# Optimization experiments

Hardware: AMD Instinct MI355X
Metric: run time of the kernel (lower is better)

## Reference

```python
import jax, jax.numpy as jnp
import numpy as np

C, N, D = 4, 300000, 128

def setup_inputs() -> dict:
    key = jax.random.key(0)
    k1, k2, k3 = jax.random.split(key, 3)
    hs = jax.random.normal(k1, (C, N, D), dtype=jnp.float32)
    # Linear(att_dim, att_dim) params (torch Linear: y = x @ W.T + b)
    W = jax.random.normal(k2, (D, D), dtype=jnp.float32) * (1.0 / np.sqrt(D))
    b = jnp.zeros((D,), dtype=jnp.float32)
    # meta attention parameter [nchannel, att_dim]
    meta_att = jax.random.normal(k3, (C, D), dtype=jnp.float32) * 0.1
    return {"hs": hs, "W": W, "b": b, "meta_att": meta_att, "nnode": N}

def reference(hs, W, b, meta_att, nnode):
    # linear_block2 applied per channel: tanh(hs @ W.T + b) -> [C, N, D]
    h = jnp.tanh(jnp.einsum('cnd,ed->cne', hs, W) + b)
    # per-channel scalar attention score: mean over nodes of h[c] . meta_att[c]
    scores = jnp.einsum('cnd,cd->c', h, meta_att) / nnode  # [C]
    att = jax.nn.softmax(scores, axis=0)                   # [C]
    # weighted sum over channels for every node (replaces per-node loop)
    aggre_hid = jnp.einsum('c,cnd->nd', att, h)            # [N, D]
    return aggre_hid
```

## Files before the change

### kernel.cpp

```cpp
#include <hip/hip_runtime.h>
#include <hip/hip_bf16.h>


#define C_CH 4
#define N_NODES 300000
#define D_DIM 128
#define M_TILE 96
#define N_TILES (N_NODES / M_TILE)
#define TILE_BYTES (M_TILE * D_DIM)
#define H_TILE_BYTES (C_CH * TILE_BYTES)

typedef short bf16x8 __attribute__((ext_vector_type(8)));
typedef float floatx4 __attribute__((ext_vector_type(4)));
typedef unsigned int uintx2 __attribute__((ext_vector_type(2)));
typedef unsigned int uintx4 __attribute__((ext_vector_type(4)));

__device__ __forceinline__ unsigned pack_bf16_rne(float a, float b) {
    unsigned ua = __builtin_bit_cast(unsigned, a);
    unsigned ub = __builtin_bit_cast(unsigned, b);
    ua += 0x7FFFu + ((ua >> 16) & 1u);
    ub += 0x7FFFu + ((ub >> 16) & 1u);
    return (ua >> 16) | (ub & 0xFFFF0000u);
}

__device__ __forceinline__ float fast_tanh(float x) {
    float ax = __builtin_fabsf(x);
    float e = __builtin_amdgcn_exp2f(ax * 2.8853900817779268f);
    float t = 1.0f - 2.0f * __builtin_amdgcn_rcpf(e + 1.0f);
    return __builtin_copysignf(t, x);
}

__device__ __forceinline__ int lds_off(int row, int d) {
    return row * 256 + ((d * 2) ^ ((row & 7) << 4));
}

__device__ __forceinline__ int t_off(int n, int e) {
    return n * 128 + (e ^ ((n & 7) << 4));
}

__device__ __forceinline__ void load_w_frags(const float* __restrict__ W,
                                             int wave, int lane, bf16x8 (&bfr)[2][4]) {
    int l15 = lane & 15, q = lane >> 4;
    #pragma unroll
    for (int et = 0; et < 2; ++et)
        #pragma unroll
        for (int s = 0; s < 4; ++s) {
            int e = wave * 32 + et * 16 + l15;
            int d0 = s * 32 + q * 8;
            const floatx4* p = reinterpret_cast<const floatx4*>(W + e * D_DIM + d0);
            floatx4 v0 = p[0], v1 = p[1];
            uintx4 u;
            u.x = pack_bf16_rne(v0.x, v0.y);
            u.y = pack_bf16_rne(v0.z, v0.w);
            u.z = pack_bf16_rne(v1.x, v1.y);
            u.w = pack_bf16_rne(v1.z, v1.w);
            bfr[et][s] = __builtin_bit_cast(bf16x8, u);
        }
}

__global__ __launch_bounds__(256, 4) void score_kernel(
        const float* __restrict__ hs, const float* __restrict__ W,
        const float* __restrict__ bvec, const float* __restrict__ meta,
        unsigned char* __restrict__ h8, float* __restrict__ partials) {
    __shared__ short As[M_TILE * D_DIM];
    __shared__ float red[4];
    int c = blockIdx.x, tile = blockIdx.y, tid = threadIdx.x;
    int wave = tid >> 6, lane = tid & 63;
    int l15 = lane & 15, q = lane >> 4;

    bf16x8 bfr[2][4];
    load_w_frags(W, wave, lane, bfr);

    const float* src = hs + (size_t)c * N_NODES * D_DIM + (size_t)tile * M_TILE * D_DIM;
    #pragma unroll
    for (int j = 0; j < 12; ++j) {
        int qq = j * 256 + tid;
        floatx4 v = __builtin_nontemporal_load(reinterpret_cast<const floatx4*>(src) + qq);
        int row = qq >> 5, d0 = (qq & 31) * 4;
        uintx2 w;
        w.x = pack_bf16_rne(v.x, v.y);
        w.y = pack_bf16_rne(v.z, v.w);
        *reinterpret_cast<uintx2*>(reinterpret_cast<char*>(As) + lds_off(row, d0)) = w;
    }
    __syncthreads();

    floatx4 acc[6][2];
    #pragma unroll
    for (int mt = 0; mt < 6; ++mt)
        #pragma unroll
        for (int et = 0; et < 2; ++et)
            acc[mt][et] = (floatx4){0.f, 0.f, 0.f, 0.f};

    #pragma unroll
    for (int s = 0; s < 4; ++s) {
        int d0 = s * 32 + q * 8;
        bf16x8 a[6];
        #pragma unroll
        for (int mt = 0; mt < 6; ++mt)
            a[mt] = *reinterpret_cast<const bf16x8*>(
                        reinterpret_cast<const char*>(As) + lds_off(mt * 16 + l15, d0));
        #pragma unroll
        for (int mt = 0; mt < 6; ++mt)
            #pragma unroll
            for (int et = 0; et < 2; ++et)
                acc[mt][et] = __builtin_amdgcn_mfma_f32_16x16x32_bf16(bfr[et][s], a[mt], acc[mt][et], 0, 0, 0);
    }

    floatx4 bvv[2], mvv[2];
    #pragma unroll
    for (int et = 0; et < 2; ++et) {
        int e0 = wave * 32 + et * 16 + q * 4;
        bvv[et] = *reinterpret_cast<const floatx4*>(bvec + e0);
        mvv[et] = *reinterpret_cast<const floatx4*>(meta + c * D_DIM + e0);
    }
    unsigned pk[6][2];
    float p = 0.f;
    #pragma unroll
    for (int mt = 0; mt < 6; ++mt)
        #pragma unroll
        for (int et = 0; et < 2; ++et) {
            unsigned u = 0;
            #pragma unroll
            for (int r = 0; r < 4; ++r) {
                float hv = fast_tanh(acc[mt][et][r] + bvv[et][r]);
                p += hv * mvv[et][r];
                int iq = (int)__builtin_rintf(hv * 127.0f);
                u |= ((unsigned)iq & 0xFFu) << (8 * r);
            }
            pk[mt][et] = u;
        }

    __syncthreads();
    char* tb = reinterpret_cast<char*>(As);
    #pragma unroll
    for (int mt = 0; mt < 6; ++mt)
        #pragma unroll
        for (int et = 0; et < 2; ++et) {
            int n = mt * 16 + l15;
            int e0 = wave * 32 + et * 16 + q * 4;
            *reinterpret_cast<unsigned*>(tb + t_off(n, e0)) = pk[mt][et];
        }
    __syncthreads();

    unsigned char* dst = h8 + (size_t)tile * H_TILE_BYTES + c * TILE_BYTES + tid * 48;
    #pragma unroll
    for (int i = 0; i < 3; ++i) {
        int g = tid * 48 + i * 16;
        int n = g >> 7, e = g & 127;
        uintx4 v = *reinterpret_cast<const uintx4*>(tb + t_off(n, e));
        *reinterpret_cast<uintx4*>(dst + i * 16) = v;
    }

    #pragma unroll
    for (int off = 32; off > 0; off >>= 1) p += __shfl_down(p, off);
    if (lane == 0) red[wave] = p;
    __syncthreads();
    if (tid == 0) partials[c * N_TILES + tile] = red[0] + red[1] + red[2] + red[3];
}

__global__ void softmax_kernel(const float* __restrict__ partials, float* __restrict__ att_out) {
    __shared__ float red[16];
    __shared__ float totals[C_CH];
    int tid = threadIdx.x;
    int wave = tid >> 6, lane = tid & 63;
    for (int c = 0; c < C_CH; ++c) {
        float s = 0.f;
        for (int i = tid; i < N_TILES; i += 1024) s += partials[c * N_TILES + i];
        #pragma unroll
        for (int off = 32; off > 0; off >>= 1) s += __shfl_down(s, off);
        if (lane == 0) red[wave] = s;
        __syncthreads();
        if (tid == 0) {
            float t = 0.f;
            #pragma unroll
            for (int w = 0; w < 16; ++w) t += red[w];
            totals[c] = t;
        }
        __syncthreads();
    }
    if (tid == 0) {
        float sc[C_CH], m = -1e30f;
        #pragma unroll
        for (int c = 0; c < C_CH; ++c) {
            sc[c] = totals[c] / (float)N_NODES;
            m = fmaxf(m, sc[c]);
        }
        float sum = 0.f;
        #pragma unroll
        for (int c = 0; c < C_CH; ++c) {
            sc[c] = __builtin_amdgcn_exp2f((sc[c] - m) * 1.4426950408889634f);
            sum += sc[c];
        }
        #pragma unroll
        for (int c = 0; c < C_CH; ++c) att_out[c] = sc[c] / sum;
    }
}

__global__ __launch_bounds__(256, 8) void combine_kernel(
        const unsigned char* __restrict__ h8, const float* __restrict__ att,
        float* __restrict__ out) {
    int tile = N_TILES - 1 - blockIdx.x;
    int tid = threadIdx.x;
    float av[C_CH];
    #pragma unroll
    for (int c = 0; c < C_CH; ++c) av[c] = att[c] * (1.0f / 127.0f);

    const unsigned char* base = h8 + (size_t)tile * H_TILE_BYTES;
    float* obase = out + (size_t)tile * (M_TILE * D_DIM);

    #pragma unroll
    for (int j = 0; j < 6; ++j) {
        int idx = j * 2048 + tid * 8;
        float sum[8];
        #pragma unroll
        for (int i = 0; i < 8; ++i) sum[i] = 0.f;
        #pragma unroll
        for (int c = 0; c < C_CH; ++c) {
            uintx2 u = *reinterpret_cast<const uintx2*>(base + c * TILE_BYTES + idx);
            #pragma unroll
            for (int i = 0; i < 4; ++i) {
                int b0 = (int)(u.x << (24 - 8 * i)) >> 24;
                int b1 = (int)(u.y << (24 - 8 * i)) >> 24;
                sum[i]     += av[c] * (float)b0;
                sum[i + 4] += av[c] * (float)b1;
            }
        }
        floatx4 o0 = {sum[0], sum[1], sum[2], sum[3]};
        floatx4 o1 = {sum[4], sum[5], sum[6], sum[7]};
        __builtin_nontemporal_store(o0, reinterpret_cast<floatx4*>(obase + idx));
        __builtin_nontemporal_store(o1, reinterpret_cast<floatx4*>(obase + idx + 4));
    }
}

extern "C" void kernel_launch(void* const* d_in, const int* in_sizes, int n_in,
                              void* d_out, int out_size, void* d_ws, size_t ws_size,
                              hipStream_t stream) {
    (void)in_sizes; (void)n_in; (void)out_size; (void)ws_size;
    const float* hs   = (const float*)d_in[0];
    const float* W    = (const float*)d_in[1];
    const float* bv   = (const float*)d_in[2];
    const float* meta = (const float*)d_in[3];
    unsigned char* h8 = (unsigned char*)d_ws;
    float* partials = (float*)((char*)d_ws + 153600000);
    float* att      = partials + C_CH * N_TILES;
    float* out      = (float*)d_out;

    score_kernel<<<dim3(C_CH, N_TILES), 256, 0, stream>>>(hs, W, bv, meta, h8, partials);
    softmax_kernel<<<1, 1024, 0, stream>>>(partials, att);
    combine_kernel<<<N_TILES, 256, 0, stream>>>(h8, att, out);
}
```

Before: 236.0 us.

## Process all channels per block with register prefetch of next channel tile

The score kernel now handles all four channels of a node tile in one block. While the MFMA and tanh work runs on the current channel, the next channel's hs tile is prefetched into registers. W fragments and the bias are loaded once per block instead of once per channel, and the quantized output gets its own LDS buffer. This is meant to hide global load latency and cut per-block setup, at the cost of more registers, more LDS and lower occupancy (launch bounds drop to 3) with four times fewer blocks.

Result: slower. 267.2 us (+13.2%).

```diff
diff --git a/kernel.cpp b/kernel.cpp
--- a/kernel.cpp
+++ b/kernel.cpp
@@ -58,104 +58,117 @@
         }
 }
 
-__global__ __launch_bounds__(256, 4) void score_kernel(
+__global__ __launch_bounds__(256, 3) void score_kernel(
         const float* __restrict__ hs, const float* __restrict__ W,
         const float* __restrict__ bvec, const float* __restrict__ meta,
         unsigned char* __restrict__ h8, float* __restrict__ partials) {
     __shared__ short As[M_TILE * D_DIM];
-    __shared__ float red[4];
-    int c = blockIdx.x, tile = blockIdx.y, tid = threadIdx.x;
+    __shared__ char  Ts[M_TILE * D_DIM];
+    __shared__ float red[4][C_CH];
+    int tile = blockIdx.x, tid = threadIdx.x;
     int wave = tid >> 6, lane = tid & 63;
     int l15 = lane & 15, q = lane >> 4;
 
     bf16x8 bfr[2][4];
     load_w_frags(W, wave, lane, bfr);
 
-    const float* src = hs + (size_t)c * N_NODES * D_DIM + (size_t)tile * M_TILE * D_DIM;
-    #pragma unroll
-    for (int j = 0; j < 12; ++j) {
-        int qq = j * 256 + tid;
-        floatx4 v = __builtin_nontemporal_load(reinterpret_cast<const floatx4*>(src) + qq);
-        int row = qq >> 5, d0 = (qq & 31) * 4;
-        uintx2 w;
-        w.x = pack_bf16_rne(v.x, v.y);
-        w.y = pack_bf16_rne(v.z, v.w);
-        *reinterpret_cast<uintx2*>(reinterpret_cast<char*>(As) + lds_off(row, d0)) = w;
+    floatx4 bvv[2];
+    #pragma unroll
+    for (int et = 0; et < 2; ++et)
+        bvv[et] = *reinterpret_cast<const floatx4*>(bvec + wave * 32 + et * 16 + q * 4);
+
+    const float* srcbase = hs + (size_t)tile * M_TILE * D_DIM;
+    floatx4 R[12];
+    #pragma unroll
+    for (int j = 0; j < 12; ++j)
+        R[j] = __builtin_nontemporal_load(reinterpret_cast<const floatx4*>(srcbase) + j * 256 + tid);
+
+    float p[C_CH];
+
+    for (int c = 0; c < C_CH; ++c) {
+        #pragma unroll
+        for (int j = 0; j < 12; ++j) {
+            int qq = j * 256 + tid;
+            int row = qq >> 5, d0 = (qq & 31) * 4;
+            uintx2 w;
+            w.x = pack_bf16_rne(R[j].x, R[j].y);
+            w.y = pack_bf16_rne(R[j].z, R[j].w);
+            *reinterpret_cast<uintx2*>(reinterpret_cast<char*>(As) + lds_off(row, d0)) = w;
+        }
+        __syncthreads();
+
+        if (c < C_CH - 1) {
+            const float* nsrc = srcbase + (size_t)(c + 1) * N_NODES * D_DIM;
+            #pragma unroll
+            for (int j = 0; j < 12; ++j)
+                R[j] = __builtin_nontemporal_load(reinterpret_cast<const floatx4*>(nsrc) + j * 256 + tid);
+        }
+
+        floatx4 acc[6][2];
+        #pragma unroll
+        for (int mt = 0; mt < 6; ++mt)
+            #pragma unroll
+            for (int et = 0; et < 2; ++et)
+                acc[mt][et] = (floatx4){0.f, 0.f, 0.f, 0.f};
+        #pragma unroll
+        for (int s = 0; s < 4; ++s) {
+            int d0 = s * 32 + q * 8;
+            bf16x8 a[6];
+            #pragma unroll
+            for (int mt = 0; mt < 6; ++mt)
+                a[mt] = *reinterpret_cast<const bf16x8*>(
+                            reinterpret_cast<const char*>(As) + lds_off(mt * 16 + l15, d0));
+            #pragma unroll
+            for (int mt = 0; mt < 6; ++mt)
+                #pragma unroll
+                for (int et = 0; et < 2; ++et)
+                    acc[mt][et] = __builtin_amdgcn_mfma_f32_16x16x32_bf16(bfr[et][s], a[mt], acc[mt][et], 0, 0, 0);
+        }
+
+        floatx4 mvv[2];
+        #pragma unroll
+        for (int et = 0; et < 2; ++et)
+            mvv[et] = *reinterpret_cast<const floatx4*>(meta + c * D_DIM + wave * 32 + et * 16 + q * 4);
+        float pc = 0.f;
+        #pragma unroll
+        for (int mt = 0; mt < 6; ++mt)
+            #pragma unroll
+            for (int et = 0; et < 2; ++et) {
+                int n = mt * 16 + l15;
+                int e0 = wave * 32 + et * 16 + q * 4;
+                unsigned u = 0;
+                #pragma unroll
+                for (int r = 0; r < 4; ++r) {
+                    float hv = fast_tanh(acc[mt][et][r] + bvv[et][r]);
+                    pc += hv * mvv[et][r];
+                    int iq = (int)__builtin_rintf(hv * 127.0f);
+                    u |= ((unsigned)iq & 0xFFu) << (8 * r);
+                }
+                *reinterpret_cast<unsigned*>(Ts + t_off(n, e0)) = u;
+            }
+        p[c] = pc;
+        __syncthreads();
+
+        unsigned char* dst = h8 + (size_t)tile * H_TILE_BYTES + c * TILE_BYTES + tid * 48;
+        #pragma unroll
+        for (int i = 0; i < 3; ++i) {
+            int g = tid * 48 + i * 16;
+            int n = g >> 7, e = g & 127;
+            uintx4 v = *reinterpret_cast<const uintx4*>(Ts + t_off(n, e));
+            *reinterpret_cast<uintx4*>(dst + i * 16) = v;
+        }
+    }
+
+    #pragma unroll
+    for (int c = 0; c < C_CH; ++c) {
+        float s = p[c];
+        #pragma unroll
+        for (int off = 32; off > 0; off >>= 1) s += __shfl_down(s, off);
+        if (lane == 0) red[wave][c] = s;
     }
     __syncthreads();
-
-    floatx4 acc[6][2];
-    #pragma unroll
-    for (int mt = 0; mt < 6; ++mt)
-        #pragma unroll
-        for (int et = 0; et < 2; ++et)
-            acc[mt][et] = (floatx4){0.f, 0.f, 0.f, 0.f};
-
-    #pragma unroll
-    for (int s = 0; s < 4; ++s) {
-        int d0 = s * 32 + q * 8;
-        bf16x8 a[6];
-        #pragma unroll
-        for (int mt = 0; mt < 6; ++mt)
-            a[mt] = *reinterpret_cast<const bf16x8*>(
-                        reinterpret_cast<const char*>(As) + lds_off(mt * 16 + l15, d0));
-        #pragma unroll
-        for (int mt = 0; mt < 6; ++mt)
-            #pragma unroll
-            for (int et = 0; et < 2; ++et)
-                acc[mt][et] = __builtin_amdgcn_mfma_f32_16x16x32_bf16(bfr[et][s], a[mt], acc[mt][et], 0, 0, 0);
-    }
-
-    floatx4 bvv[2], mvv[2];
-    #pragma unroll
-    for (int et = 0; et < 2; ++et) {
-        int e0 = wave * 32 + et * 16 + q * 4;
-        bvv[et] = *reinterpret_cast<const floatx4*>(bvec + e0);
-        mvv[et] = *reinterpret_cast<const floatx4*>(meta + c * D_DIM + e0);
-    }
-    unsigned pk[6][2];
-    float p = 0.f;
-    #pragma unroll
-    for (int mt = 0; mt < 6; ++mt)
-        #pragma unroll
-        for (int et = 0; et < 2; ++et) {
-            unsigned u = 0;
-            #pragma unroll
-            for (int r = 0; r < 4; ++r) {
-                float hv = fast_tanh(acc[mt][et][r] + bvv[et][r]);
-                p += hv * mvv[et][r];
-                int iq = (int)__builtin_rintf(hv * 127.0f);
-                u |= ((unsigned)iq & 0xFFu) << (8 * r);
-            }
-            pk[mt][et] = u;
-        }
-
-    __syncthreads();
-    char* tb = reinterpret_cast<char*>(As);
-    #pragma unroll
-    for (int mt = 0; mt < 6; ++mt)
-        #pragma unroll
-        for (int et = 0; et < 2; ++et) {
-            int n = mt * 16 + l15;
-            int e0 = wave * 32 + et * 16 + q * 4;
-            *reinterpret_cast<unsigned*>(tb + t_off(n, e0)) = pk[mt][et];
-        }
-    __syncthreads();
-
-    unsigned char* dst = h8 + (size_t)tile * H_TILE_BYTES + c * TILE_BYTES + tid * 48;
-    #pragma unroll
-    for (int i = 0; i < 3; ++i) {
-        int g = tid * 48 + i * 16;
-        int n = g >> 7, e = g & 127;
-        uintx4 v = *reinterpret_cast<const uintx4*>(tb + t_off(n, e));
-        *reinterpret_cast<uintx4*>(dst + i * 16) = v;
-    }
-
-    #pragma unroll
-    for (int off = 32; off > 0; off >>= 1) p += __shfl_down(p, off);
-    if (lane == 0) red[wave] = p;
-    __syncthreads();
-    if (tid == 0) partials[c * N_TILES + tile] = red[0] + red[1] + red[2] + red[3];
+    if (tid < C_CH)
+        partials[tid * N_TILES + tile] = red[0][tid] + red[1][tid] + red[2][tid] + red[3][tid];
 }
 
 __global__ void softmax_kernel(const float* __restrict__ partials, float* __restrict__ att_out) {
@@ -245,7 +258,7 @@
     float* att      = partials + C_CH * N_TILES;
     float* out      = (float*)d_out;
 
-    score_kernel<<<dim3(C_CH, N_TILES), 256, 0, stream>>>(hs, W, bv, meta, h8, partials);
+    score_kernel<<<N_TILES, 256, 0, stream>>>(hs, W, bv, meta, h8, partials);
     softmax_kernel<<<1, 1024, 0, stream>>>(partials, att);
     combine_kernel<<<N_TILES, 256, 0, stream>>>(h8, att, out);
 }
```
